# Kernel tuning notes

Measured on AMD Instinct MI355X. Metric: run time of the kernel, lower is better.

## Reference

```python
import jax, jax.numpy as jnp
import numpy as np

K = 7          # involution kernel size
PAD = 3        # (K-1)//2
G = 4          # groups = out_channels // group_channels
GC = 16        # group_channels
EPS = 1e-5     # BatchNorm eps


def _bn(x, g, b, m, v):
    # eval-mode BatchNorm2d over channel dim of NCHW
    scale = g / jnp.sqrt(v + EPS)
    return x * scale[:, None, None] + (b - m * scale)[:, None, None]


def _conv1x1(x, w, b=None):
    y = jnp.einsum('bchw,oc->bohw', x, w)
    if b is not None:
        y = y + b[:, None, None]
    return y


def _gelu(x):
    return jax.nn.gelu(x, approximate=False)  # torch nn.GELU default (erf)


def _involution(x, wr, gr, br, mr, vr, ws, bs):
    # kernel-generation branch: 1x1 reduce -> BN -> ReLU -> 1x1 span
    r = jax.nn.relu(_bn(_conv1x1(x, wr), gr, br, mr, vr))
    w = _conv1x1(r, ws, bs)                       # [B, G*K*K, H, W]
    B, _, H, W = w.shape
    w = w.reshape(B, G, K * K, H, W)
    # unfold x into KxK patches (channel-major then row-major kernel pos, matching nn.Unfold)
    xp = jnp.pad(x, ((0, 0), (0, 0), (PAD, PAD), (PAD, PAD)))
    patches = jnp.stack([xp[:, :, i:i + H, j:j + W]
                         for i in range(K) for j in range(K)], axis=2)  # [B, C, KK, H, W]
    patches = patches.reshape(B, G, GC, K * K, H, W)
    out = jnp.einsum('bgkhw,bgckhw->bgchw', w, patches)  # per-pixel dynamic kernel apply
    return out.reshape(B, G * GC, H, W)


def setup_inputs() -> dict:
    key = jax.random.key(0)
    ks = jax.random.split(key, 24)
    B, Cin, Cout, H, W = 4, 32, 64, 128, 128
    red = Cout // 4
    n = lambda k, s, sc: jax.random.normal(k, s, jnp.float32) * sc
    u = lambda k, s: jax.random.uniform(k, s, jnp.float32, 0.5, 1.5)
    inp = {
        'x': n(ks[0], (B, Cin, H, W), 1.0),
        'w1': n(ks[1], (Cout, Cin), 0.15),
        # involution: reduce conv + BN, span conv
        'wr': n(ks[2], (red, Cout), 0.12), 'gr': u(ks[3], (red,)), 'br': n(ks[4], (red,), 0.05),
        'mr': n(ks[5], (red,), 0.05), 'vr': u(ks[6], (red,)),
        'ws': n(ks[7], (K * K * G, red), 0.1), 'bs': n(ks[8], (K * K * G,), 0.02),
        # BN after involution
        'g1': u(ks[9], (Cout,)), 'b1': n(ks[10], (Cout,), 0.05),
        'm1': n(ks[11], (Cout,), 0.05), 'v1': u(ks[12], (Cout,)),
        # convblock2
        'w2': n(ks[13], (Cout, Cout), 0.12),
        'g2': u(ks[14], (Cout,)), 'b2': n(ks[15], (Cout,), 0.05),
        'm2': n(ks[16], (Cout,), 0.05), 'v2': u(ks[17], (Cout,)),
        # mapping (residual projection) conv has bias=True by default
        'wm': n(ks[18], (Cout, Cin), 0.15), 'bmap': n(ks[19], (Cout,), 0.02),
        'gm': u(ks[20], (Cout,)), 'betam': n(ks[21], (Cout,), 0.05),
        'mm': n(ks[22], (Cout,), 0.05), 'vm': u(ks[23], (Cout,)),
    }
    return inp


def reference(x, w1, wr, gr, br, mr, vr, ws, bs, g1, b1, m1, v1,
              w2, g2, b2, m2, v2, wm, bmap, gm, betam, mm, vm):
    x1 = _gelu(_conv1x1(x, w1))                                  # convblock
    x1 = _gelu(_bn(_involution(x1, wr, gr, br, mr, vr, ws, bs),
                   g1, b1, m1, v1))                              # involution + BN + GELU
    x1 = _bn(_conv1x1(x1, w2), g2, b2, m2, v2)                   # convblock2
    skip = _bn(_conv1x1(x, wm, bmap), gm, betam, mm, vm)         # mapping (Cin != Cout)
    return _gelu(x1 + skip)
```

## Files before the change

### kernel.cpp

```cpp
#include <hip/hip_runtime.h>
#include <hip/hip_bf16.h>
#include <math.h>

#define HW    16384
#define Bsz   4
#define CIN   32
#define COUT  64
#define RED   16
#define KKN   49
#define GG    4
#define PW    134
#define PPLANE (PW*PW)
#define NHALO 25152

typedef __hip_bfloat16 bf16;
typedef __attribute__((ext_vector_type(8))) short bf16x8;
typedef __attribute__((ext_vector_type(4))) float f32x4;

__device__ __forceinline__ float gelu_f(float x) {
    return 0.5f * x * (1.0f + erff(x * 0.70710678118654752f));
}
__device__ __forceinline__ void unpack_bf2(unsigned u, float& lo, float& hi) {
    lo = __uint_as_float(u << 16);
    hi = __uint_as_float(u & 0xffff0000u);
}
__device__ __forceinline__ unsigned pack_bf2(float lo, float hi) {
    unsigned a = __float_as_uint(lo), b = __float_as_uint(hi);
    a += 0x7fff + ((a >> 16) & 1);
    b += 0x7fff + ((b >> 16) & 1);
    return (a >> 16) | (b & 0xffff0000u);
}
__device__ __forceinline__ unsigned short bf16r(float v) {
    unsigned a = __float_as_uint(v);
    a += 0x7fff + ((a >> 16) & 1);
    return (unsigned short)(a >> 16);
}

#define OFF_RBUF  9437184
#define OFF_X2B   13631488
#define OFF_PAR   22020096
#define OFF_XBF   22085632
#define PRSH_F 0
#define PSHC_F 16
#define PSMV_F 80
#define PSC1_F 144
#define PSH1_F 208
#define BW1B 4096
#define BWRB 8192
#define BCAT 12288

__global__ __launch_bounds__(256) void k0_init(
    const float* __restrict__ x,
    const float* __restrict__ w1, const float* __restrict__ wr,
    const float* __restrict__ gr, const float* __restrict__ br,
    const float* __restrict__ mr, const float* __restrict__ vr,
    const float* __restrict__ g1, const float* __restrict__ b1,
    const float* __restrict__ m1, const float* __restrict__ v1,
    const float* __restrict__ w2, const float* __restrict__ g2,
    const float* __restrict__ b2, const float* __restrict__ m2,
    const float* __restrict__ v2,
    const float* __restrict__ wm, const float* __restrict__ bmap,
    const float* __restrict__ gm, const float* __restrict__ betam,
    const float* __restrict__ mm, const float* __restrict__ vm,
    char* __restrict__ parb, uint4* __restrict__ x1pad,
    unsigned short* __restrict__ xbf, int nzb)
{
    int bid = blockIdx.x, t = threadIdx.x;
    if (bid >= 1 && bid <= nzb) {
        unsigned i = (unsigned)(bid - 1) * 256u + (unsigned)t;
        if (i < NHALO) {
            unsigned plane = i / 1572u;
            unsigned rem = i - plane * 1572u;
            unsigned row, col;
            if (rem < 804u) {
                unsigned rr = rem / 134u;
                col = rem - rr * 134u;
                row = rr < 3u ? rr : rr + 128u;
            } else {
                unsigned r2 = rem - 804u;
                unsigned rr = r2 / 6u;
                unsigned cc = r2 - rr * 6u;
                row = rr + 3u;
                col = cc < 3u ? cc : cc + 128u;
            }
            uint4* q = x1pad + ((size_t)(plane * PW + row) * PW + col) * 2;
            q[0] = make_uint4(0u, 0u, 0u, 0u);
            q[1] = make_uint4(0u, 0u, 0u, 0u);
        }
        return;
    }
    if (bid > nzb) {
        int gpx = (bid - nzb - 1) * 256 + t;
        int b = gpx >> 14, p = gpx & (HW - 1);
        float xv[CIN];
#pragma unroll
        for (int c = 0; c < CIN; ++c) xv[c] = x[(b * CIN + c) * HW + p];
        unsigned pk[16];
#pragma unroll
        for (int d = 0; d < 16; ++d) pk[d] = pack_bf2(xv[2 * d], xv[2 * d + 1]);
        unsigned* xo = (unsigned*)&xbf[(size_t)gpx * 32];
        *(uint4*)xo        = make_uint4(pk[0], pk[1], pk[2], pk[3]);
        *(uint4*)(xo + 4)  = make_uint4(pk[4], pk[5], pk[6], pk[7]);
        *(uint4*)(xo + 8)  = make_uint4(pk[8], pk[9], pk[10], pk[11]);
        *(uint4*)(xo + 12) = make_uint4(pk[12], pk[13], pk[14], pk[15]);
        return;
    }
    float* parf = (float*)parb;
    unsigned short* w1b  = (unsigned short*)(parb + BW1B);
    unsigned short* wrb  = (unsigned short*)(parb + BWRB);
    unsigned short* wcat = (unsigned short*)(parb + BCAT);
    for (int i = t; i < 64 * 32; i += 256)
        w1b[i] = bf16r(w1[i]);
    for (int i = t; i < 16 * 64; i += 256) {
        int j = i >> 6;
        float sc = gr[j] * rsqrtf(vr[j] + 1e-5f);
        wrb[i] = bf16r(wr[i] * sc);
    }
    for (int i = t; i < 64 * 96; i += 256) {
        int o = i / 96, c = i - o * 96;
        float v;
        if (c < 64) {
            float s2 = g2[o] * rsqrtf(v2[o] + 1e-5f);
            float sm = gm[o] * rsqrtf(vm[o] + 1e-5f);
            v = w2[o * COUT + c] * (s2 / sm);
        } else {
            v = wm[o * CIN + (c - 64)];
        }
        wcat[i] = bf16r(v);
    }
    if (t < 16) {
        float sc = gr[t] * rsqrtf(vr[t] + 1e-5f);
        parf[PRSH_F + t] = br[t] - mr[t] * sc;
    }
    if (t < 64) {
        float s2 = g2[t] * rsqrtf(v2[t] + 1e-5f);
        float sm = gm[t] * rsqrtf(vm[t] + 1e-5f);
        parf[PSHC_F + t] = (b2[t] - m2[t] * s2) + (betam[t] + (bmap[t] - mm[t]) * sm);
        parf[PSMV_F + t] = sm;
        float s1 = g1[t] * rsqrtf(v1[t] + 1e-5f);
        parf[PSC1_F + t] = s1;
        parf[PSH1_F + t] = b1[t] - m1[t] * s1;
    }
}

__global__ __launch_bounds__(256, 4) void k1_mfma(
    const unsigned short* __restrict__ xbf, const char* __restrict__ parb,
    unsigned* __restrict__ x1pad, float* __restrict__ rbuf)
{
    __shared__ float x1f[4][16][65];

    int lane = threadIdx.x & 63;
    int wave = threadIdx.x >> 6;
    int m15 = lane & 15, quad = lane >> 4;
    int base_gpx = blockIdx.x * 64 + wave * 16;
    int b   = base_gpx >> 14;
    int px0 = base_gpx & (HW - 1);

    const unsigned short* w1b = (const unsigned short*)(parb + BW1B);
    const unsigned short* wrb = (const unsigned short*)(parb + BWRB);
    const float* parf = (const float*)parb;

    bf16x8 Af = *(const bf16x8*)&xbf[((size_t)(base_gpx + m15)) * 32 + quad * 8];
    f32x4 acc[4];
#pragma unroll
    for (int nt = 0; nt < 4; ++nt) {
        bf16x8 Bf = *(const bf16x8*)&w1b[(nt * 16 + m15) * 32 + quad * 8];
        f32x4 z = {0.f, 0.f, 0.f, 0.f};
        acc[nt] = __builtin_amdgcn_mfma_f32_16x16x32_bf16(Af, Bf, z, 0, 0, 0);
    }
#pragma unroll
    for (int nt = 0; nt < 4; ++nt)
#pragma unroll
        for (int reg = 0; reg < 4; ++reg)
            x1f[wave][quad * 4 + reg][nt * 16 + m15] = gelu_f(acc[nt][reg]);

    __syncthreads();

    {
        int pxl = lane >> 2, g = lane & 3;
        int p = px0 + pxl, h = p >> 7, w = p & 127;
        unsigned pk[8];
#pragma unroll
        for (int d = 0; d < 8; ++d)
            pk[d] = pack_bf2(x1f[wave][pxl][g * 16 + 2 * d],
                             x1f[wave][pxl][g * 16 + 2 * d + 1]);
        unsigned* xo = x1pad +
            ((size_t)((b * GG + g) * PW + (h + 3)) * PW + (w + 3)) * 8;
        *(uint4*)xo       = make_uint4(pk[0], pk[1], pk[2], pk[3]);
        *(uint4*)(xo + 4) = make_uint4(pk[4], pk[5], pk[6], pk[7]);
    }

    f32x4 racc = {0.f, 0.f, 0.f, 0.f};
#pragma unroll
    for (int kt = 0; kt < 2; ++kt) {
        bf16x8 A2, B2;
#pragma unroll
        for (int j = 0; j < 8; ++j)
            A2[j] = (short)bf16r(x1f[wave][m15][kt * 32 + quad * 8 + j]);
        B2 = *(const bf16x8*)&wrb[m15 * 64 + kt * 32 + quad * 8];
        racc = __builtin_amdgcn_mfma_f32_16x16x32_bf16(A2, B2, racc, 0, 0, 0);
    }
    float rsh = parf[PRSH_F + m15];
#pragma unroll
    for (int reg = 0; reg < 4; ++reg) {
        int gp = base_gpx + quad * 4 + reg;
        rbuf[(size_t)gp * 16 + m15] = fmaxf(racc[reg] + rsh, 0.f);
    }
}

__global__ __launch_bounds__(256, 4) void k34_fused(
    const unsigned* __restrict__ x1pad, const float* __restrict__ rbuf,
    const float* __restrict__ wsp, const float* __restrict__ bsp,
    const char* __restrict__ parb, const unsigned short* __restrict__ xbf,
    float* __restrict__ out)
{
    __shared__ unsigned short x2t[64][88];

    const float* par = (const float*)parb;
    int t = threadIdx.x;
    int b = blockIdx.x >> 8;
    int pxblk = (blockIdx.x & 255) << 6;

    {
        int pxl = t & 63;
        int g = __builtin_amdgcn_readfirstlane(t >> 6);
        int p = pxblk + pxl;
        int h = p >> 7, w0 = p & 127;
        int bg = b * GG + g;

        float r[RED];
        {
            const float4* rp = (const float4*)&rbuf[((size_t)b * HW + p) * 16];
            float4 r0 = rp[0], r1 = rp[1], r2 = rp[2], r3 = rp[3];
            r[0]=r0.x; r[1]=r0.y; r[2]=r0.z; r[3]=r0.w;
            r[4]=r1.x; r[5]=r1.y; r[6]=r1.z; r[7]=r1.w;
            r[8]=r2.x; r[9]=r2.y; r[10]=r2.z; r[11]=r2.w;
            r[12]=r3.x; r[13]=r3.y; r[14]=r3.z; r[15]=r3.w;
        }

        const float* wrow = wsp + g * KKN * RED;
        const float* brow = bsp + g * KKN;
        const unsigned* base = x1pad + ((size_t)(bg * PW + h) * PW + w0) * 8;

        float acc[RED];
#pragma unroll
        for (int c = 0; c < RED; ++c) acc[c] = 0.f;

#pragma unroll 1
        for (int i = 0; i < 7; ++i) {
#pragma unroll 1
            for (int j = 0; j < 7; ++j) {
                int k = i * 7 + j;
                const float* wk_row = wrow + k * RED;
                float s = brow[k];
#pragma unroll
                for (int jj = 0; jj < RED; ++jj) s += r[jj] * wk_row[jj];
                const unsigned* tp = base + (size_t)(i * PW + j) * 8;
                uint4 A = *(const uint4*)tp;
                uint4 B = *(const uint4*)(tp + 4);
                float lo, hi;
                unpack_bf2(A.x, lo, hi); acc[0] += s*lo; acc[1] += s*hi;
                unpack_bf2(A.y, lo, hi); acc[2] += s*lo; acc[3] += s*hi;
                unpack_bf2(A.z, lo, hi); acc[4] += s*lo; acc[5] += s*hi;
                unpack_bf2(A.w, lo, hi); acc[6] += s*lo; acc[7] += s*hi;
                unpack_bf2(B.x, lo, hi); acc[8] += s*lo; acc[9] += s*hi;
                unpack_bf2(B.y, lo, hi); acc[10]+= s*lo; acc[11]+= s*hi;
                unpack_bf2(B.z, lo, hi); acc[12]+= s*lo; acc[13]+= s*hi;
                unpack_bf2(B.w, lo, hi); acc[14]+= s*lo; acc[15]+= s*hi;
            }
        }

        unsigned pk[8];
#pragma unroll
        for (int d = 0; d < 8; ++d) {
            int ch0 = g * RED + 2 * d, ch1 = ch0 + 1;
            float v0 = gelu_f(par[PSC1_F + ch0] * acc[2 * d]     + par[PSH1_F + ch0]);
            float v1 = gelu_f(par[PSC1_F + ch1] * acc[2 * d + 1] + par[PSH1_F + ch1]);
            pk[d] = pack_bf2(v0, v1);
        }
        unsigned* xo = (unsigned*)&x2t[pxl][g * RED];
        *(uint4*)xo       = make_uint4(pk[0], pk[1], pk[2], pk[3]);
        *(uint4*)(xo + 4) = make_uint4(pk[4], pk[5], pk[6], pk[7]);
    }

    __syncthreads();

    {
        int lane = t & 63, wave = t >> 6;
        int m15  = lane & 15;
        int quad = lane >> 4;
        int pxl0 = wave * 16;
        int px0  = pxblk + pxl0;

        const unsigned short* wcat = (const unsigned short*)(parb + BCAT);

        bf16x8 Bf[3][4];
#pragma unroll
        for (int kt = 0; kt < 3; ++kt)
#pragma unroll
            for (int nt = 0; nt < 4; ++nt)
                Bf[kt][nt] = *(const bf16x8*)&wcat[(nt * 16 + m15) * 96 + kt * 32 + quad * 8];

        bf16x8 Af[3];
        Af[0] = *(const bf16x8*)&x2t[pxl0 + m15][quad * 8];
        Af[1] = *(const bf16x8*)&x2t[pxl0 + m15][32 + quad * 8];
        Af[2] = *(const bf16x8*)&xbf[((size_t)(b * HW + px0 + m15)) * 32 + quad * 8];

        f32x4 acc[4];
#pragma unroll
        for (int nt = 0; nt < 4; ++nt) acc[nt] = (f32x4){0.f, 0.f, 0.f, 0.f};
#pragma unroll
        for (int kt = 0; kt < 3; ++kt)
#pragma unroll
            for (int nt = 0; nt < 4; ++nt)
                acc[nt] = __builtin_amdgcn_mfma_f32_16x16x32_bf16(
                    Af[kt], Bf[kt][nt], acc[nt], 0, 0, 0);

#pragma unroll
        for (int nt = 0; nt < 4; ++nt) {
            int o = nt * 16 + m15;
            float smv = par[PSMV_F + o], sh = par[PSHC_F + o];
            float* op = out + (size_t)(b * COUT + o) * HW + px0 + quad * 4;
#pragma unroll
            for (int reg = 0; reg < 4; ++reg)
                op[reg] = gelu_f(smv * acc[nt][reg] + sh);
        }
    }
}

extern "C" void kernel_launch(void* const* d_in, const int* in_sizes, int n_in,
                              void* d_out, int out_size, void* d_ws, size_t ws_size,
                              hipStream_t stream) {
    const float* x    = (const float*)d_in[0];
    const float* w1   = (const float*)d_in[1];
    const float* wr   = (const float*)d_in[2];
    const float* gr   = (const float*)d_in[3];
    const float* br   = (const float*)d_in[4];
    const float* mr   = (const float*)d_in[5];
    const float* vr   = (const float*)d_in[6];
    const float* wsp  = (const float*)d_in[7];
    const float* bsp  = (const float*)d_in[8];
    const float* g1   = (const float*)d_in[9];
    const float* b1   = (const float*)d_in[10];
    const float* m1   = (const float*)d_in[11];
    const float* v1   = (const float*)d_in[12];
    const float* w2   = (const float*)d_in[13];
    const float* g2   = (const float*)d_in[14];
    const float* b2   = (const float*)d_in[15];
    const float* m2   = (const float*)d_in[16];
    const float* v2   = (const float*)d_in[17];
    const float* wm   = (const float*)d_in[18];
    const float* bmap = (const float*)d_in[19];
    const float* gm   = (const float*)d_in[20];
    const float* betam= (const float*)d_in[21];
    const float* mm   = (const float*)d_in[22];
    const float* vm   = (const float*)d_in[23];

    unsigned*       x1pad = (unsigned*)d_ws;
    float*          rbuf  = (float*)((char*)d_ws + OFF_RBUF);
    char*           parb  = (char*)d_ws + OFF_PAR;
    unsigned short* xbf   = (unsigned short*)((char*)d_ws + OFF_XBF);

    int nzb = (NHALO + 255) / 256;
    int nxb = Bsz * HW / 256;
    k0_init<<<1 + nzb + nxb, 256, 0, stream>>>(
        x, w1, wr, gr, br, mr, vr, g1, b1, m1, v1,
        w2, g2, b2, m2, v2, wm, bmap, gm, betam, mm, vm,
        parb, (uint4*)x1pad, xbf, nzb);
    k1_mfma<<<Bsz * HW / 64, 256, 0, stream>>>(xbf, parb, x1pad, rbuf);
    k34_fused<<<Bsz * GG * HW / 256, 256, 0, stream>>>(
        x1pad, rbuf, wsp, bsp, parb, xbf, (float*)d_out);
}
```

Baseline: 166.1 us.

## Merge init into first kernel and compute two output rows per thread in involution

```diff
diff --git a/kernel.cpp b/kernel.cpp
--- a/kernel.cpp
+++ b/kernel.cpp
@@ -10,8 +10,9 @@
 #define KKN   49
 #define GG    4
 #define PW    134
-#define PPLANE (PW*PW)
 #define NHALO 25152
+#define NZB   99
+#define NPXB  1024
 
 typedef __hip_bfloat16 bf16;
 typedef __attribute__((ext_vector_type(8))) short bf16x8;
@@ -37,23 +38,19 @@
 }
 
 #define OFF_RBUF  9437184
-#define OFF_X2B   13631488
 #define OFF_PAR   22020096
 #define OFF_XBF   22085632
-#define PRSH_F 0
 #define PSHC_F 16
 #define PSMV_F 80
 #define PSC1_F 144
 #define PSH1_F 208
-#define BW1B 4096
-#define BWRB 8192
 #define BCAT 12288
 
-__global__ __launch_bounds__(256) void k0_init(
-    const float* __restrict__ x,
-    const float* __restrict__ w1, const float* __restrict__ wr,
-    const float* __restrict__ gr, const float* __restrict__ br,
-    const float* __restrict__ mr, const float* __restrict__ vr,
+__global__ __launch_bounds__(256, 4) void k1_all(
+    const float* __restrict__ x, const float* __restrict__ w1,
+    const float* __restrict__ wr, const float* __restrict__ gr,
+    const float* __restrict__ br, const float* __restrict__ mr,
+    const float* __restrict__ vr,
     const float* __restrict__ g1, const float* __restrict__ b1,
     const float* __restrict__ m1, const float* __restrict__ v1,
     const float* __restrict__ w2, const float* __restrict__ g2,
@@ -62,111 +59,98 @@
     const float* __restrict__ wm, const float* __restrict__ bmap,
     const float* __restrict__ gm, const float* __restrict__ betam,
     const float* __restrict__ mm, const float* __restrict__ vm,
-    char* __restrict__ parb, uint4* __restrict__ x1pad,
-    unsigned short* __restrict__ xbf, int nzb)
-{
-    int bid = blockIdx.x, t = threadIdx.x;
-    if (bid >= 1 && bid <= nzb) {
-        unsigned i = (unsigned)(bid - 1) * 256u + (unsigned)t;
-        if (i < NHALO) {
-            unsigned plane = i / 1572u;
-            unsigned rem = i - plane * 1572u;
-            unsigned row, col;
-            if (rem < 804u) {
-                unsigned rr = rem / 134u;
-                col = rem - rr * 134u;
-                row = rr < 3u ? rr : rr + 128u;
-            } else {
-                unsigned r2 = rem - 804u;
-                unsigned rr = r2 / 6u;
-                unsigned cc = r2 - rr * 6u;
-                row = rr + 3u;
-                col = cc < 3u ? cc : cc + 128u;
-            }
-            uint4* q = x1pad + ((size_t)(plane * PW + row) * PW + col) * 2;
-            q[0] = make_uint4(0u, 0u, 0u, 0u);
-            q[1] = make_uint4(0u, 0u, 0u, 0u);
-        }
-        return;
-    }
-    if (bid > nzb) {
-        int gpx = (bid - nzb - 1) * 256 + t;
-        int b = gpx >> 14, p = gpx & (HW - 1);
-        float xv[CIN];
-#pragma unroll
-        for (int c = 0; c < CIN; ++c) xv[c] = x[(b * CIN + c) * HW + p];
-        unsigned pk[16];
-#pragma unroll
-        for (int d = 0; d < 16; ++d) pk[d] = pack_bf2(xv[2 * d], xv[2 * d + 1]);
-        unsigned* xo = (unsigned*)&xbf[(size_t)gpx * 32];
-        *(uint4*)xo        = make_uint4(pk[0], pk[1], pk[2], pk[3]);
-        *(uint4*)(xo + 4)  = make_uint4(pk[4], pk[5], pk[6], pk[7]);
-        *(uint4*)(xo + 8)  = make_uint4(pk[8], pk[9], pk[10], pk[11]);
-        *(uint4*)(xo + 12) = make_uint4(pk[12], pk[13], pk[14], pk[15]);
-        return;
-    }
-    float* parf = (float*)parb;
-    unsigned short* w1b  = (unsigned short*)(parb + BW1B);
-    unsigned short* wrb  = (unsigned short*)(parb + BWRB);
-    unsigned short* wcat = (unsigned short*)(parb + BCAT);
-    for (int i = t; i < 64 * 32; i += 256)
-        w1b[i] = bf16r(w1[i]);
-    for (int i = t; i < 16 * 64; i += 256) {
-        int j = i >> 6;
-        float sc = gr[j] * rsqrtf(vr[j] + 1e-5f);
-        wrb[i] = bf16r(wr[i] * sc);
-    }
-    for (int i = t; i < 64 * 96; i += 256) {
-        int o = i / 96, c = i - o * 96;
-        float v;
-        if (c < 64) {
-            float s2 = g2[o] * rsqrtf(v2[o] + 1e-5f);
-            float sm = gm[o] * rsqrtf(vm[o] + 1e-5f);
-            v = w2[o * COUT + c] * (s2 / sm);
-        } else {
-            v = wm[o * CIN + (c - 64)];
-        }
-        wcat[i] = bf16r(v);
-    }
-    if (t < 16) {
-        float sc = gr[t] * rsqrtf(vr[t] + 1e-5f);
-        parf[PRSH_F + t] = br[t] - mr[t] * sc;
-    }
-    if (t < 64) {
-        float s2 = g2[t] * rsqrtf(v2[t] + 1e-5f);
-        float sm = gm[t] * rsqrtf(vm[t] + 1e-5f);
-        parf[PSHC_F + t] = (b2[t] - m2[t] * s2) + (betam[t] + (bmap[t] - mm[t]) * sm);
-        parf[PSMV_F + t] = sm;
-        float s1 = g1[t] * rsqrtf(v1[t] + 1e-5f);
-        parf[PSC1_F + t] = s1;
-        parf[PSH1_F + t] = b1[t] - m1[t] * s1;
-    }
-}
-
-__global__ __launch_bounds__(256, 4) void k1_mfma(
-    const unsigned short* __restrict__ xbf, const char* __restrict__ parb,
-    unsigned* __restrict__ x1pad, float* __restrict__ rbuf)
+    char* __restrict__ parb, unsigned* __restrict__ x1pad,
+    unsigned short* __restrict__ xbf, float* __restrict__ rbuf)
 {
     __shared__ float x1f[4][16][65];
-
-    int lane = threadIdx.x & 63;
-    int wave = threadIdx.x >> 6;
+    int bid = blockIdx.x, t = threadIdx.x;
+
+    if (bid >= NPXB) {
+        int hb = bid - NPXB;
+        if (hb < NZB) {
+            unsigned i = (unsigned)hb * 256u + (unsigned)t;
+            if (i < NHALO) {
+                unsigned plane = i / 1572u;
+                unsigned rem = i - plane * 1572u;
+                unsigned row, col;
+                if (rem < 804u) {
+                    unsigned rr = rem / 134u;
+                    col = rem - rr * 134u;
+                    row = rr < 3u ? rr : rr + 128u;
+                } else {
+                    unsigned r2 = rem - 804u;
+                    unsigned rr = r2 / 6u;
+                    unsigned cc = r2 - rr * 6u;
+                    row = rr + 3u;
+                    col = cc < 3u ? cc : cc + 128u;
+                }
+                uint4* q = (uint4*)x1pad + ((size_t)(plane * PW + row) * PW + col) * 2;
+                q[0] = make_uint4(0u, 0u, 0u, 0u);
+                q[1] = make_uint4(0u, 0u, 0u, 0u);
+            }
+        } else {
+            float* parf = (float*)parb;
+            unsigned short* wcat = (unsigned short*)(parb + BCAT);
+            for (int i = t; i < 64 * 96; i += 256) {
+                int o = i / 96, c = i - o * 96;
+                float v;
+                if (c < 64) {
+                    float s2 = g2[o] * rsqrtf(v2[o] + 1e-5f);
+                    float sm = gm[o] * rsqrtf(vm[o] + 1e-5f);
+                    v = w2[o * COUT + c] * (s2 / sm);
+                } else {
+                    v = wm[o * CIN + (c - 64)];
+                }
+                wcat[i] = bf16r(v);
+            }
+            if (t < 64) {
+                float s2 = g2[t] * rsqrtf(v2[t] + 1e-5f);
+                float sm = gm[t] * rsqrtf(vm[t] + 1e-5f);
+                parf[PSHC_F + t] = (b2[t] - m2[t] * s2) + (betam[t] + (bmap[t] - mm[t]) * sm);
+                parf[PSMV_F + t] = sm;
+                float s1 = g1[t] * rsqrtf(v1[t] + 1e-5f);
+                parf[PSC1_F + t] = s1;
+                parf[PSH1_F + t] = b1[t] - m1[t] * s1;
+            }
+        }
+        return;
+    }
+
+    int lane = t & 63;
+    int wave = t >> 6;
     int m15 = lane & 15, quad = lane >> 4;
-    int base_gpx = blockIdx.x * 64 + wave * 16;
+    int base_gpx = bid * 64 + wave * 16;
     int b   = base_gpx >> 14;
     int px0 = base_gpx & (HW - 1);
 
-    const unsigned short* w1b = (const unsigned short*)(parb + BW1B);
-    const unsigned short* wrb = (const unsigned short*)(parb + BWRB);
-    const float* parf = (const float*)parb;
-
-    bf16x8 Af = *(const bf16x8*)&xbf[((size_t)(base_gpx + m15)) * 32 + quad * 8];
+    int gpx = base_gpx + m15;
+    int p   = gpx & (HW - 1);
+    unsigned apk[4];
+#pragma unroll
+    for (int d = 0; d < 4; ++d) {
+        float lo = x[((size_t)(b * CIN + quad * 8 + 2 * d)) * HW + p];
+        float hi = x[((size_t)(b * CIN + quad * 8 + 2 * d + 1)) * HW + p];
+        apk[d] = pack_bf2(lo, hi);
+    }
+    union BU { uint4 q; bf16x8 v; };
+    BU au; au.q = make_uint4(apk[0], apk[1], apk[2], apk[3]);
+    bf16x8 Af = au.v;
+    *(uint4*)&xbf[(size_t)gpx * 32 + quad * 8] = au.q;
+
     f32x4 acc[4];
 #pragma unroll
     for (int nt = 0; nt < 4; ++nt) {
-        bf16x8 Bf = *(const bf16x8*)&w1b[(nt * 16 + m15) * 32 + quad * 8];
+        int o = nt * 16 + m15;
+        unsigned bpk[4];
+#pragma unroll
+        for (int d = 0; d < 4; ++d) {
+            float lo = w1[o * CIN + quad * 8 + 2 * d];
+            float hi = w1[o * CIN + quad * 8 + 2 * d + 1];
+            bpk[d] = pack_bf2(lo, hi);
+        }
+        BU bu; bu.q = make_uint4(bpk[0], bpk[1], bpk[2], bpk[3]);
         f32x4 z = {0.f, 0.f, 0.f, 0.f};
-        acc[nt] = __builtin_amdgcn_mfma_f32_16x16x32_bf16(Af, Bf, z, 0, 0, 0);
+        acc[nt] = __builtin_amdgcn_mfma_f32_16x16x32_bf16(Af, bu.v, z, 0, 0, 0);
     }
 #pragma unroll
     for (int nt = 0; nt < 4; ++nt)
@@ -178,7 +162,7 @@
 
     {
         int pxl = lane >> 2, g = lane & 3;
-        int p = px0 + pxl, h = p >> 7, w = p & 127;
+        int pp = px0 + pxl, h = pp >> 7, w = pp & 127;
         unsigned pk[8];
 #pragma unroll
         for (int d = 0; d < 8; ++d)
@@ -190,17 +174,19 @@
         *(uint4*)(xo + 4) = make_uint4(pk[4], pk[5], pk[6], pk[7]);
     }
 
+    float sc  = gr[m15] * rsqrtf(vr[m15] + 1e-5f);
+    float rsh = br[m15] - mr[m15] * sc;
     f32x4 racc = {0.f, 0.f, 0.f, 0.f};
 #pragma unroll
     for (int kt = 0; kt < 2; ++kt) {
         bf16x8 A2, B2;
 #pragma unroll
-        for (int j = 0; j < 8; ++j)
+        for (int j = 0; j < 8; ++j) {
             A2[j] = (short)bf16r(x1f[wave][m15][kt * 32 + quad * 8 + j]);
-        B2 = *(const bf16x8*)&wrb[m15 * 64 + kt * 32 + quad * 8];
+            B2[j] = (short)bf16r(wr[m15 * 64 + kt * 32 + quad * 8 + j] * sc);
+        }
         racc = __builtin_amdgcn_mfma_f32_16x16x32_bf16(A2, B2, racc, 0, 0, 0);
     }
-    float rsh = parf[PRSH_F + m15];
 #pragma unroll
     for (int reg = 0; reg < 4; ++reg) {
         int gp = base_gpx + quad * 4 + reg;
@@ -208,79 +194,104 @@
     }
 }
 
-__global__ __launch_bounds__(256, 4) void k34_fused(
+__global__ __launch_bounds__(256, 2) void k34_fused(
     const unsigned* __restrict__ x1pad, const float* __restrict__ rbuf,
     const float* __restrict__ wsp, const float* __restrict__ bsp,
     const char* __restrict__ parb, const unsigned short* __restrict__ xbf,
     float* __restrict__ out)
 {
-    __shared__ unsigned short x2t[64][88];
+    __shared__ unsigned short x2t[2][64][88];
 
     const float* par = (const float*)parb;
     int t = threadIdx.x;
-    int b = blockIdx.x >> 8;
-    int pxblk = (blockIdx.x & 255) << 6;
+    int b    = blockIdx.x >> 7;
+    int tile = blockIdx.x & 127;
+    int R  = tile >> 1;
+    int Cc = tile & 1;
+    int h0 = 2 * R;
 
     {
-        int pxl = t & 63;
+        int c = t & 63;
         int g = __builtin_amdgcn_readfirstlane(t >> 6);
-        int p = pxblk + pxl;
-        int h = p >> 7, w0 = p & 127;
+        int w0 = Cc * 64 + c;
+        int p0 = h0 * 128 + w0;
         int bg = b * GG + g;
 
-        float r[RED];
+        float r0[RED], r1[RED];
         {
-            const float4* rp = (const float4*)&rbuf[((size_t)b * HW + p) * 16];
-            float4 r0 = rp[0], r1 = rp[1], r2 = rp[2], r3 = rp[3];
-            r[0]=r0.x; r[1]=r0.y; r[2]=r0.z; r[3]=r0.w;
-            r[4]=r1.x; r[5]=r1.y; r[6]=r1.z; r[7]=r1.w;
-            r[8]=r2.x; r[9]=r2.y; r[10]=r2.z; r[11]=r2.w;
-            r[12]=r3.x; r[13]=r3.y; r[14]=r3.z; r[15]=r3.w;
+            const float4* rp = (const float4*)&rbuf[((size_t)b * HW + p0) * 16];
+            float4 a0 = rp[0], a1 = rp[1], a2 = rp[2], a3 = rp[3];
+            r0[0]=a0.x; r0[1]=a0.y; r0[2]=a0.z; r0[3]=a0.w;
+            r0[4]=a1.x; r0[5]=a1.y; r0[6]=a1.z; r0[7]=a1.w;
+            r0[8]=a2.x; r0[9]=a2.y; r0[10]=a2.z; r0[11]=a2.w;
+            r0[12]=a3.x; r0[13]=a3.y; r0[14]=a3.z; r0[15]=a3.w;
+            const float4* rq = (const float4*)&rbuf[((size_t)b * HW + p0 + 128) * 16];
+            float4 c0 = rq[0], c1 = rq[1], c2 = rq[2], c3 = rq[3];
+            r1[0]=c0.x; r1[1]=c0.y; r1[2]=c0.z; r1[3]=c0.w;
+            r1[4]=c1.x; r1[5]=c1.y; r1[6]=c1.z; r1[7]=c1.w;
+            r1[8]=c2.x; r1[9]=c2.y; r1[10]=c2.z; r1[11]=c2.w;
+            r1[12]=c3.x; r1[13]=c3.y; r1[14]=c3.z; r1[15]=c3.w;
         }
 
         const float* wrow = wsp + g * KKN * RED;
         const float* brow = bsp + g * KKN;
-        const unsigned* base = x1pad + ((size_t)(bg * PW + h) * PW + w0) * 8;
-
-        float acc[RED];
-#pragma unroll
-        for (int c = 0; c < RED; ++c) acc[c] = 0.f;
+
+        float acc0[RED], acc1[RED];
+#pragma unroll
+        for (int cc = 0; cc < RED; ++cc) { acc0[cc] = 0.f; acc1[cc] = 0.f; }
 
 #pragma unroll 1
-        for (int i = 0; i < 7; ++i) {
+        for (int ir = 0; ir < 8; ++ir) {
+            const unsigned* rowp = x1pad +
+                ((size_t)(bg * PW + h0 + ir) * PW + w0) * 8;
 #pragma unroll 1
             for (int j = 0; j < 7; ++j) {
-                int k = i * 7 + j;
-                const float* wk_row = wrow + k * RED;
-                float s = brow[k];
-#pragma unroll
-                for (int jj = 0; jj < RED; ++jj) s += r[jj] * wk_row[jj];
-                const unsigned* tp = base + (size_t)(i * PW + j) * 8;
+                const unsigned* tp = rowp + (size_t)j * 8;
                 uint4 A = *(const uint4*)tp;
                 uint4 B = *(const uint4*)(tp + 4);
-                float lo, hi;
-                unpack_bf2(A.x, lo, hi); acc[0] += s*lo; acc[1] += s*hi;
-                unpack_bf2(A.y, lo, hi); acc[2] += s*lo; acc[3] += s*hi;
-                unpack_bf2(A.z, lo, hi); acc[4] += s*lo; acc[5] += s*hi;
-                unpack_bf2(A.w, lo, hi); acc[6] += s*lo; acc[7] += s*hi;
-                unpack_bf2(B.x, lo, hi); acc[8] += s*lo; acc[9] += s*hi;
-                unpack_bf2(B.y, lo, hi); acc[10]+= s*lo; acc[11]+= s*hi;
-                unpack_bf2(B.z, lo, hi); acc[12]+= s*lo; acc[13]+= s*hi;
-                unpack_bf2(B.w, lo, hi); acc[14]+= s*lo; acc[15]+= s*hi;
-            }
-        }
-
-        unsigned pk[8];
+                float f[16];
+                unpack_bf2(A.x, f[0], f[1]);   unpack_bf2(A.y, f[2], f[3]);
+                unpack_bf2(A.z, f[4], f[5]);   unpack_bf2(A.w, f[6], f[7]);
+                unpack_bf2(B.x, f[8], f[9]);   unpack_bf2(B.y, f[10], f[11]);
+                unpack_bf2(B.z, f[12], f[13]); unpack_bf2(B.w, f[14], f[15]);
+                if (ir < 7) {
+                    int k = ir * 7 + j;
+                    const float* wk = wrow + k * RED;
+                    float s = brow[k];
+#pragma unroll
+                    for (int jj = 0; jj < RED; ++jj) s += r0[jj] * wk[jj];
+#pragma unroll
+                    for (int cc = 0; cc < RED; ++cc) acc0[cc] += s * f[cc];
+                }
+                if (ir > 0) {
+                    int k = (ir - 1) * 7 + j;
+                    const float* wk = wrow + k * RED;
+                    float s = brow[k];
+#pragma unroll
+                    for (int jj = 0; jj < RED; ++jj) s += r1[jj] * wk[jj];
+#pragma unroll
+                    for (int cc = 0; cc < RED; ++cc) acc1[cc] += s * f[cc];
+                }
+            }
+        }
+
+        unsigned pk0[8], pk1[8];
 #pragma unroll
         for (int d = 0; d < 8; ++d) {
             int ch0 = g * RED + 2 * d, ch1 = ch0 + 1;
-            float v0 = gelu_f(par[PSC1_F + ch0] * acc[2 * d]     + par[PSH1_F + ch0]);
-            float v1 = gelu_f(par[PSC1_F + ch1] * acc[2 * d + 1] + par[PSH1_F + ch1]);
-            pk[d] = pack_bf2(v0, v1);
-        }
-        unsigned* xo = (unsigned*)&x2t[pxl][g * RED];
-        *(uint4*)xo       = make_uint4(pk[0], pk[1], pk[2], pk[3]);
-        *(uint4*)(xo + 4) = make_uint4(pk[4], pk[5], pk[6], pk[7]);
+            float sA = par[PSC1_F + ch0], sB = par[PSC1_F + ch1];
+            float hA = par[PSH1_F + ch0], hB = par[PSH1_F + ch1];
+            pk0[d] = pack_bf2(gelu_f(sA * acc0[2 * d]     + hA),
+                              gelu_f(sB * acc0[2 * d + 1] + hB));
+            pk1[d] = pack_bf2(gelu_f(sA * acc1[2 * d]     + hA),
+                              gelu_f(sB * acc1[2 * d + 1] + hB));
+        }
+        unsigned* xo0 = (unsigned*)&x2t[0][c][g * RED];
+        *(uint4*)xo0       = make_uint4(pk0[0], pk0[1], pk0[2], pk0[3]);
+        *(uint4*)(xo0 + 4) = make_uint4(pk0[4], pk0[5], pk0[6], pk0[7]);
+        unsigned* xo1 = (unsigned*)&x2t[1][c][g * RED];
+        *(uint4*)xo1       = make_uint4(pk1[0], pk1[1], pk1[2], pk1[3]);
+        *(uint4*)(xo1 + 4) = make_uint4(pk1[4], pk1[5], pk1[6], pk1[7]);
     }
 
     __syncthreads();
@@ -290,7 +301,6 @@
         int m15  = lane & 15;
         int quad = lane >> 4;
         int pxl0 = wave * 16;
-        int px0  = pxblk + pxl0;
 
         const unsigned short* wcat = (const unsigned short*)(parb + BCAT);
 
@@ -301,29 +311,34 @@
             for (int nt = 0; nt < 4; ++nt)
                 Bf[kt][nt] = *(const bf16x8*)&wcat[(nt * 16 + m15) * 96 + kt * 32 + quad * 8];
 
-        bf16x8 Af[3];
-        Af[0] = *(const bf16x8*)&x2t[pxl0 + m15][quad * 8];
-        Af[1] = *(const bf16x8*)&x2t[pxl0 + m15][32 + quad * 8];
-        Af[2] = *(const bf16x8*)&xbf[((size_t)(b * HW + px0 + m15)) * 32 + quad * 8];
-
-        f32x4 acc[4];
-#pragma unroll
-        for (int nt = 0; nt < 4; ++nt) acc[nt] = (f32x4){0.f, 0.f, 0.f, 0.f};
-#pragma unroll
-        for (int kt = 0; kt < 3; ++kt)
-#pragma unroll
-            for (int nt = 0; nt < 4; ++nt)
-                acc[nt] = __builtin_amdgcn_mfma_f32_16x16x32_bf16(
-                    Af[kt], Bf[kt][nt], acc[nt], 0, 0, 0);
-
-#pragma unroll
-        for (int nt = 0; nt < 4; ++nt) {
-            int o = nt * 16 + m15;
-            float smv = par[PSMV_F + o], sh = par[PSHC_F + o];
-            float* op = out + (size_t)(b * COUT + o) * HW + px0 + quad * 4;
-#pragma unroll
-            for (int reg = 0; reg < 4; ++reg)
-                op[reg] = gelu_f(smv * acc[nt][reg] + sh);
+#pragma unroll 1
+        for (int rr = 0; rr < 2; ++rr) {
+            int pbase = (h0 + rr) * 128 + Cc * 64;
+
+            bf16x8 Af[3];
+            Af[0] = *(const bf16x8*)&x2t[rr][pxl0 + m15][quad * 8];
+            Af[1] = *(const bf16x8*)&x2t[rr][pxl0 + m15][32 + quad * 8];
+            Af[2] = *(const bf16x8*)&xbf[((size_t)(b * HW + pbase + pxl0 + m15)) * 32 + quad * 8];
+
+            f32x4 acc[4];
+#pragma unroll
+            for (int nt = 0; nt < 4; ++nt) acc[nt] = (f32x4){0.f, 0.f, 0.f, 0.f};
+#pragma unroll
+            for (int kt = 0; kt < 3; ++kt)
+#pragma unroll
+                for (int nt = 0; nt < 4; ++nt)
+                    acc[nt] = __builtin_amdgcn_mfma_f32_16x16x32_bf16(
+                        Af[kt], Bf[kt][nt], acc[nt], 0, 0, 0);
+
+#pragma unroll
+            for (int nt = 0; nt < 4; ++nt) {
+                int o = nt * 16 + m15;
+                float smv = par[PSMV_F + o], sh = par[PSHC_F + o];
+                float* op = out + (size_t)(b * COUT + o) * HW + pbase + pxl0 + quad * 4;
+#pragma unroll
+                for (int reg = 0; reg < 4; ++reg)
+                    op[reg] = gelu_f(smv * acc[nt][reg] + sh);
+            }
         }
     }
 }
@@ -361,13 +376,10 @@
     char*           parb  = (char*)d_ws + OFF_PAR;
     unsigned short* xbf   = (unsigned short*)((char*)d_ws + OFF_XBF);
 
-    int nzb = (NHALO + 255) / 256;
-    int nxb = Bsz * HW / 256;
-    k0_init<<<1 + nzb + nxb, 256, 0, stream>>>(
+    k1_all<<<NPXB + NZB + 1, 256, 0, stream>>>(
         x, w1, wr, gr, br, mr, vr, g1, b1, m1, v1,
         w2, g2, b2, m2, v2, wm, bmap, gm, betam, mm, vm,
-        parb, (uint4*)x1pad, xbf, nzb);
-    k1_mfma<<<Bsz * HW / 64, 256, 0, stream>>>(xbf, parb, x1pad, rbuf);
-    k34_fused<<<Bsz * GG * HW / 256, 256, 0, stream>>>(
+        parb, x1pad, xbf, rbuf);
+    k34_fused<<<Bsz * (HW / 128), 256, 0, stream>>>(
         x1pad, rbuf, wsp, bsp, parb, xbf, (float*)d_out);
 }
```

Result: slower. 169.8 us (+2.2%).
